# Kernel tuning notes

Hardware: AMD Instinct MI355X
Metric: run time of the kernel (lower is better)

The kernel has to match this reference:

```python
import jax, jax.numpy as jnp
import numpy as np

NUM_USERS = 200000
NUM_ARTISTS = 50000
LATENT_DIM = 64
NUM_EDGES = 2000000
NUM_LAYERS = 3


def setup_inputs() -> dict:
    key = jax.random.key(0)
    k_u, k_a, k_src, k_dst = jax.random.split(key, 4)
    x_users = jax.random.normal(k_u, (NUM_USERS, LATENT_DIM), dtype=jnp.float32)
    x_artists = jax.random.normal(k_a, (NUM_ARTISTS, LATENT_DIM), dtype=jnp.float32)
    # a2u: row 0 = artist (source) ids, row 1 = user (target) ids
    art = jax.random.randint(k_src, (NUM_EDGES,), 0, NUM_ARTISTS, dtype=jnp.int32)
    usr = jax.random.randint(k_dst, (NUM_EDGES,), 0, NUM_USERS, dtype=jnp.int32)
    edge_index_a2u = jnp.stack([art, usr], axis=0)
    # u2a is the reversed edge list: row 0 = user (source), row 1 = artist (target)
    edge_index_u2a = jnp.stack([usr, art], axis=0)
    return {
        "x_users": x_users,
        "x_artists": x_artists,
        "edge_index_a2u": edge_index_a2u,
        "edge_index_u2a": edge_index_u2a,
    }


def _scatter_mean(src_nodes, edge_index, dim_size):
    """Gather src_nodes[edge_index[0]] and scatter-mean onto edge_index[1].

    Matches torch_scatter.scatter(reduce='mean'): empty segments yield 0.
    """
    msgs = src_nodes[edge_index[0]]                     # [E, D] gather
    sums = jax.ops.segment_sum(msgs, edge_index[1], num_segments=dim_size)
    ones = jnp.ones((edge_index.shape[1],), dtype=src_nodes.dtype)
    counts = jax.ops.segment_sum(ones, edge_index[1], num_segments=dim_size)
    return sums / jnp.maximum(counts, 1.0)[:, None]


def reference(x_users, x_artists, edge_index_a2u, edge_index_u2a):
    scale = 1.0 / (NUM_LAYERS + 1)
    final_u = x_users * scale
    final_a = x_artists * scale
    for _ in range(NUM_LAYERS):
        x_users = _scatter_mean(x_artists, edge_index_a2u, NUM_USERS)
        x_artists = _scatter_mean(x_users, edge_index_u2a, NUM_ARTISTS)
        final_u = final_u + x_users * scale
        final_a = final_a + x_artists * scale
    return final_u, final_a
```

## Files before the change

### kernel.cpp

```cpp
#include <hip/hip_runtime.h>
#include <hip/hip_fp16.h>

#define D 64
#define TB 256

#define BSHIFT_U 10
#define BSHIFT_A 8
#define CAP    12288
#define CAPC_U 16384
#define CAPC_A 12288
#define TSHIFT 14
#define PCHUNK 4096

typedef _Float16 half8 __attribute__((ext_vector_type(8)));
typedef float float8 __attribute__((ext_vector_type(8)));
typedef float f32x4 __attribute__((ext_vector_type(4)));

__device__ __forceinline__ float8 h8_to_f8(half8 h) {
    return __builtin_convertvector(h, float8);
}
template <typename T>
__device__ __forceinline__ T ntl(const T* p) { return __builtin_nontemporal_load(p); }
template <typename T>
__device__ __forceinline__ void nts(T* p, T v) { __builtin_nontemporal_store(v, p); }

__global__ __launch_bounds__(TB) void cvt_f16_kernel(const f32x4* __restrict__ in,
                                                     half8* __restrict__ out, int n8) {
    int i = blockIdx.x * blockDim.x + threadIdx.x;
    int stride = gridDim.x * blockDim.x;
    for (int j = i; j < n8; j += stride) {
        f32x4 a = in[j * 2 + 0];
        f32x4 b = in[j * 2 + 1];
        half8 h;
        h[0] = (_Float16)a[0]; h[1] = (_Float16)a[1]; h[2] = (_Float16)a[2]; h[3] = (_Float16)a[3];
        h[4] = (_Float16)b[0]; h[5] = (_Float16)b[1]; h[6] = (_Float16)b[2]; h[7] = (_Float16)b[3];
        out[j] = h;
    }
}

struct PartShared {
    unsigned recs[PCHUNK];
    unsigned sorted[PCHUNK];
    unsigned short loc[PCHUNK];
    unsigned char bkt[PCHUNK];
    int cnt[256];
    int gbase[256];
    int seg[256];
    int scanbuf[TB];
};

__device__ __forceinline__ void part_direction(PartShared& sh, int m, int NB,
                                               int* __restrict__ bcur,
                                               unsigned* __restrict__ part) {
    const int tid = threadIdx.x;
    for (int i = tid; i < NB; i += TB) sh.cnt[i] = 0;
    __syncthreads();
    for (int i = tid; i < m; i += TB)
        sh.loc[i] = (unsigned short)atomicAdd(&sh.cnt[sh.bkt[i]], 1);
    __syncthreads();
    int v = (tid < NB) ? sh.cnt[tid] : 0;
    sh.scanbuf[tid] = v;
    __syncthreads();
    for (int off = 1; off < TB; off <<= 1) {
        int t = (tid >= off) ? sh.scanbuf[tid - off] : 0;
        __syncthreads();
        if (tid >= off) sh.scanbuf[tid] += t;
        __syncthreads();
    }
    if (tid < NB) {
        sh.seg[tid] = sh.scanbuf[tid] - v;
        if (v) sh.gbase[tid] = atomicAdd(&bcur[tid], v);
    }
    __syncthreads();
    for (int i = tid; i < m; i += TB)
        sh.sorted[sh.seg[sh.bkt[i]] + sh.loc[i]] = sh.recs[i];
    __syncthreads();
    const int wid = tid >> 6;
    const int lane = tid & 63;
    for (int b = wid; b < NB; b += TB / 64) {
        int s = sh.seg[b];
        int send = (b + 1 < NB) ? sh.seg[b + 1] : m;
        if (send <= s) continue;
        unsigned* dst = part + (size_t)b * CAP + sh.gbase[b];
        for (int i = s + lane; i < send; i += 64) dst[i - s] = sh.sorted[i];
    }
    __syncthreads();
}

__global__ __launch_bounds__(TB) void partition_both_kernel(const int* __restrict__ art,
                                                            const int* __restrict__ usr, int E,
                                                            int* __restrict__ bcur_u,
                                                            int* __restrict__ bcur_a,
                                                            unsigned* __restrict__ part_u,
                                                            unsigned* __restrict__ part_a,
                                                            int NBu, int NBa) {
    __shared__ PartShared sh;
    const int tid = threadIdx.x;
    const int dir = blockIdx.x & 1;
    const int cidx = blockIdx.x >> 1;
    const int nchunks = gridDim.x >> 1;
    for (int c = cidx; (size_t)c * PCHUNK < (size_t)E; c += nchunks) {
        const int c0 = c * PCHUNK;
        const int m = min(PCHUNK, E - c0);
        if (dir == 0) {
            for (int i = tid; i < m; i += TB) {
                int a = art[c0 + i], u = usr[c0 + i];
                sh.recs[i] = ((unsigned)a << BSHIFT_U) | ((unsigned)u & ((1u << BSHIFT_U) - 1u));
                sh.bkt[i] = (unsigned char)(u >> BSHIFT_U);
            }
            __syncthreads();
            part_direction(sh, m, NBu, bcur_u, part_u);
        } else {
            for (int i = tid; i < m; i += TB) {
                int a = art[c0 + i], u = usr[c0 + i];
                sh.recs[i] = ((unsigned)u << BSHIFT_A) | ((unsigned)a & ((1u << BSHIFT_A) - 1u));
                sh.bkt[i] = (unsigned char)(a >> BSHIFT_A);
            }
            __syncthreads();
            part_direction(sh, m, NBa, bcur_a, part_a);
        }
    }
}

template <int NPB, int NB, int BSHIFT>
__device__ __forceinline__ void local_csr_body(const unsigned* __restrict__ part,
                                               int ecount, int ebeg_p, int ebeg_c, int n0,
                                               int2* __restrict__ rowdeg,
                                               int* __restrict__ csr, int N,
                                               int* cnt, int* sdata) {
    const int tid = threadIdx.x;
    const int NBINS = NPB * NB;
    const int eend = ebeg_p + ecount;
    const unsigned mask = (unsigned)(NPB - 1);
    for (int i = tid; i < NBINS; i += TB) cnt[i] = 0;
    __syncthreads();
    for (int e = ebeg_p + tid; e < eend; e += TB) {
        unsigned r = part[e];
        int bin = (int)(r & mask) * NB + (int)((r >> BSHIFT) >> TSHIFT);
        atomicAdd(&cnt[bin], 1);
    }
    __syncthreads();
    const int ITEMS = NBINS / TB;
    const int NPT = ITEMS / NB;
    const int ib = tid * ITEMS;
    int dj[NPT], pdj[NPT], nsj[NPT];
    int local = 0;
    for (int j = 0; j < NPT; ++j) {
        int d = 0;
        for (int k = 0; k < NB; ++k) d += cnt[ib + j * NB + k];
        dj[j] = d;
        pdj[j] = (d + 3) & ~3;
        local += pdj[j];
    }
    sdata[tid] = local;
    __syncthreads();
    for (int off = 1; off < TB; off <<= 1) {
        int t = (tid >= off) ? sdata[tid - off] : 0;
        __syncthreads();
        if (tid >= off) sdata[tid] += t;
        __syncthreads();
    }
    int run = sdata[tid] - local;
    for (int j = 0; j < NPT; ++j) {
        nsj[j] = run;
        int c = run;
        for (int k = 0; k < NB; ++k) {
            int idx = ib + j * NB + k;
            int v = cnt[idx];
            cnt[idx] = c;
            c += v;
        }
        int n = n0 + tid * NPT + j;
        if (n < N) rowdeg[n] = make_int2(ebeg_c + run, dj[j]);
        run += pdj[j];
    }
    __syncthreads();
    for (int e = ebeg_p + tid; e < eend; e += TB) {
        unsigned r = part[e];
        int bin = (int)(r & mask) * NB + (int)((r >> BSHIFT) >> TSHIFT);
        int pos = atomicAdd(&cnt[bin], 1);
        csr[ebeg_c + pos] = (int)(r >> BSHIFT);
    }
    for (int j = 0; j < NPT; ++j)
        for (int k = dj[j]; k < pdj[j]; ++k) csr[ebeg_c + nsj[j] + k] = 0;
}

__global__ __launch_bounds__(TB) void local_csr_both_kernel(const unsigned* __restrict__ part_u,
                                                            const unsigned* __restrict__ part_a,
                                                            const int* __restrict__ bcur_u,
                                                            const int* __restrict__ bcur_a,
                                                            int2* __restrict__ rowdeg_u,
                                                            int2* __restrict__ rowdeg_a,
                                                            int* __restrict__ csr_u,
                                                            int* __restrict__ csr_a,
                                                            int NU, int NA, int NBu) {
    __shared__ int cnt[4096];
    __shared__ int sdata[TB];
    const int b = blockIdx.x;
    if (b < NBu) {
        local_csr_body<1024, 4, BSHIFT_U>(part_u, bcur_u[b], b * CAP, b * CAPC_U,
                                          b << BSHIFT_U, rowdeg_u, csr_u, NU, cnt, sdata);
    } else {
        const int bb = b - NBu;
        local_csr_body<256, 16, BSHIFT_A>(part_a, bcur_a[bb], bb * CAP, bb * CAPC_A,
                                          bb << BSHIFT_A, rowdeg_a, csr_a, NA, cnt, sdata);
    }
}

__global__ __launch_bounds__(TB) void gather_mean_kernel(const half8* __restrict__ src,
                                                         const int* __restrict__ csr,
                                                         const int2* __restrict__ rowdeg,
                                                         half8* __restrict__ x_out,
                                                         f32x4* __restrict__ final_acc,
                                                         const f32x4* __restrict__ init_src,
                                                         const f32x4* __restrict__ fin_in0,
                                                         const half8* __restrict__ fin_x1,
                                                         const half8* __restrict__ fin_x2,
                                                         f32x4* __restrict__ fin_out,
                                                         int N, float scale) {
    const int lane = threadIdx.x & 7;
    int g = (blockIdx.x * blockDim.x + threadIdx.x) >> 3;
    const int ngroups = (gridDim.x * blockDim.x) >> 3;
    const float8 r0 = h8_to_f8(src[lane]);
    for (int n = g; n < N; n += ngroups) {
        const int2 rd = rowdeg[n];
        const int beg = rd.x;
        const int dg = rd.y;
        const int pd = (dg + 3) & ~3;
        const int end = beg + pd;
        float8 a0 = 0.f, a1 = 0.f, a2 = 0.f, a3 = 0.f;
        int e = beg;
        for (; e + 8 <= end; e += 8) {
            const int s0 = csr[e + 0];
            const int s1 = csr[e + 1];
            const int s2 = csr[e + 2];
            const int s3 = csr[e + 3];
            const int s4 = csr[e + 4];
            const int s5 = csr[e + 5];
            const int s6 = csr[e + 6];
            const int s7 = csr[e + 7];
            const half8 v0 = src[s0 * 8 + lane];
            const half8 v1 = src[s1 * 8 + lane];
            const half8 v2 = src[s2 * 8 + lane];
            const half8 v3 = src[s3 * 8 + lane];
            const half8 v4 = src[s4 * 8 + lane];
            const half8 v5 = src[s5 * 8 + lane];
            const half8 v6 = src[s6 * 8 + lane];
            const half8 v7 = src[s7 * 8 + lane];
            a0 += h8_to_f8(v0);
            a1 += h8_to_f8(v1);
            a2 += h8_to_f8(v2);
            a3 += h8_to_f8(v3);
            a0 += h8_to_f8(v4);
            a1 += h8_to_f8(v5);
            a2 += h8_to_f8(v6);
            a3 += h8_to_f8(v7);
        }
        if (e < end) {
            const int s0 = csr[e + 0];
            const int s1 = csr[e + 1];
            const int s2 = csr[e + 2];
            const int s3 = csr[e + 3];
            a0 += h8_to_f8(src[s0 * 8 + lane]);
            a1 += h8_to_f8(src[s1 * 8 + lane]);
            a2 += h8_to_f8(src[s2 * 8 + lane]);
            a3 += h8_to_f8(src[s3 * 8 + lane]);
        }
        float8 s = (a0 + a1) + (a2 + a3);
        s -= (float)(pd - dg) * r0;
        const float inv = 1.f / (float)(dg > 0 ? dg : 1);
        float8 x = s * inv;
        const int o8 = n * 8 + lane;
        if (x_out != nullptr) {
            half8 h;
            for (int k = 0; k < 8; ++k) h[k] = (_Float16)x[k];
            x_out[o8] = h;
        }
        const int fo = n * (D / 4) + lane * 2;
        if (fin_out != nullptr) {
            float8 t = h8_to_f8(ntl(&fin_x1[o8])) + h8_to_f8(ntl(&fin_x2[o8])) + x;
            f32x4 f0 = ntl(&fin_in0[fo + 0]);
            f32x4 f1 = ntl(&fin_in0[fo + 1]);
            f32x4 t0 = {t[0], t[1], t[2], t[3]};
            f32x4 t1 = {t[4], t[5], t[6], t[7]};
            nts(&fin_out[fo + 0], (f0 + t0) * scale);
            nts(&fin_out[fo + 1], (f1 + t1) * scale);
        }
        if (final_acc != nullptr) {
            f32x4 f0, f1;
            if (init_src != nullptr) {
                f0 = init_src[fo + 0] * scale;
                f1 = init_src[fo + 1] * scale;
            } else {
                f0 = final_acc[fo + 0];
                f1 = final_acc[fo + 1];
            }
            f32x4 x0 = {x[0], x[1], x[2], x[3]};
            f32x4 x1 = {x[4], x[5], x[6], x[7]};
            final_acc[fo + 0] = f0 + x0 * scale;
            final_acc[fo + 1] = f1 + x1 * scale;
        }
    }
}

extern "C" void kernel_launch(void* const* d_in, const int* in_sizes, int n_in,
                              void* d_out, int out_size, void* d_ws, size_t ws_size,
                              hipStream_t stream) {
    const float* x_users   = (const float*)d_in[0];
    const float* x_artists = (const float*)d_in[1];
    const int*   a2u       = (const int*)d_in[2];

    const int NU = in_sizes[0] / D;
    const int NA = in_sizes[1] / D;
    const int E  = in_sizes[2] / 2;
    const int* art = a2u;
    const int* usr = a2u + E;

    const float scale = 0.25f;

    const int NBu = (NU + (1 << BSHIFT_U) - 1) >> BSHIFT_U;
    const int NBa = (NA + (1 << BSHIFT_A) - 1) >> BSHIFT_A;

    char* w = (char*)d_ws;
    size_t off = 0;
    auto alloc = [&](size_t bytes) -> char* {
        char* p = w + off;
        off += (bytes + 255) & ~(size_t)255;
        return p;
    };
    int2* rowdeg_u = (int2*)alloc((size_t)NU * 8);
    int2* rowdeg_a = (int2*)alloc((size_t)NA * 8);
    int* bcur      = (int*)alloc((size_t)(NBu + NBa) * 4);
    int* bcur_u    = bcur;
    int* bcur_a    = bcur + NBu;
    int* csr_u     = (int*)alloc((size_t)NBu * CAPC_U * 4);
    int* csr_a     = (int*)alloc((size_t)NBa * CAPC_A * 4);
    half8* xa_in   = (half8*)alloc((size_t)NA * D * 2);
    unsigned* part_u = (unsigned*)alloc((size_t)NBu * CAP * 4);
    unsigned* part_a = (unsigned*)alloc((size_t)NBa * CAP * 4);

    const size_t XU = (size_t)NU * D * 2;
    const size_t XA = (size_t)NA * D * 2;
    const size_t XUa = (XU + 255) & ~(size_t)255;
    const size_t XAa = (XA + 255) & ~(size_t)255;

    const bool modeA = (off + 3 * XUa) <= ws_size;

    half8* x_u1 = (half8*)alloc(XU);
    half8* x_u2 = modeA ? (half8*)alloc(XU) : x_u1;
    half8* x_u3 = modeA ? (half8*)alloc(XU) : x_u1;
    char* part_base = (char*)part_u;
    half8* x_a1 = (half8*)(part_base);
    half8* x_a2 = modeA ? (half8*)(part_base + XAa) : x_a1;

    float* out_u = (float*)d_out;
    float* out_a = out_u + (size_t)NU * D;

    hipMemsetAsync(bcur, 0, (size_t)(NBu + NBa) * 4, stream);
    cvt_f16_kernel<<<1024, TB, 0, stream>>>((const f32x4*)x_artists, xa_in, NA * D / 8);
    const int nchunks = (E + PCHUNK - 1) / PCHUNK;
    partition_both_kernel<<<2 * nchunks, TB, 0, stream>>>(art, usr, E, bcur_u, bcur_a,
                                                          part_u, part_a, NBu, NBa);
    local_csr_both_kernel<<<NBu + NBa, TB, 0, stream>>>(part_u, part_a, bcur_u, bcur_a,
                                                        rowdeg_u, rowdeg_a,
                                                        csr_u, csr_a, NU, NA, NBu);

    half8* xu_buf[3] = {x_u1, x_u2, x_u3};
    half8* xa_buf[2] = {x_a1, x_a2};
    const half8* srcA = xa_in;
    for (int l = 0; l < 3; ++l) {
        const bool last = (l == 2);
        gather_mean_kernel<<<4096, TB, 0, stream>>>(
            srcA, csr_u, rowdeg_u, xu_buf[l],
            modeA ? nullptr : (f32x4*)out_u,
            (!modeA && l == 0) ? (const f32x4*)x_users : nullptr,
            (modeA && last) ? (const f32x4*)x_users : nullptr,
            (modeA && last) ? x_u1 : nullptr,
            (modeA && last) ? x_u2 : nullptr,
            (modeA && last) ? (f32x4*)out_u : nullptr,
            NU, scale);
        gather_mean_kernel<<<2048, TB, 0, stream>>>(
            xu_buf[l], csr_a, rowdeg_a,
            (modeA && last) ? nullptr : (modeA ? xa_buf[l] : x_a1),
            modeA ? nullptr : (f32x4*)out_a,
            (!modeA && l == 0) ? (const f32x4*)x_artists : nullptr,
            (modeA && last) ? (const f32x4*)x_artists : nullptr,
            (modeA && last) ? x_a1 : nullptr,
            (modeA && last) ? x_a2 : nullptr,
            (modeA && last) ? (f32x4*)out_a : nullptr,
            NA, scale);
        srcA = modeA ? xa_buf[l < 2 ? l : 0] : x_a1;
    }
}
```

Measured before the change: 347.3 us.

## Slim partition kernel to one chunk per block and use nontemporal CSR loads

The partition kernel now handles one smaller chunk per block instead of looping over chunks. It drops the shared recs and bkt staging arrays, recomputing bucket keys from global memory instead. This cuts shared-memory use so more blocks can be resident, at the cost of reading the edge arrays twice. The gather kernel now reads CSR indices and rowdeg with nontemporal loads so they do not pollute cache space needed for the feature gathers. The launch grid is not visible, so it must supply enough blocks to cover every chunk.

```diff
diff --git a/kernel.cpp b/kernel.cpp
--- a/kernel.cpp
+++ b/kernel.cpp
@@ -10,7 +10,7 @@
 #define CAPC_U 16384
 #define CAPC_A 12288
 #define TSHIFT 14
-#define PCHUNK 4096
+#define PCHUNK 2048
 
 typedef _Float16 half8 __attribute__((ext_vector_type(8)));
 typedef float float8 __attribute__((ext_vector_type(8)));
@@ -39,53 +39,13 @@
 }
 
 struct PartShared {
-    unsigned recs[PCHUNK];
     unsigned sorted[PCHUNK];
     unsigned short loc[PCHUNK];
-    unsigned char bkt[PCHUNK];
     int cnt[256];
     int gbase[256];
     int seg[256];
     int scanbuf[TB];
 };
-
-__device__ __forceinline__ void part_direction(PartShared& sh, int m, int NB,
-                                               int* __restrict__ bcur,
-                                               unsigned* __restrict__ part) {
-    const int tid = threadIdx.x;
-    for (int i = tid; i < NB; i += TB) sh.cnt[i] = 0;
-    __syncthreads();
-    for (int i = tid; i < m; i += TB)
-        sh.loc[i] = (unsigned short)atomicAdd(&sh.cnt[sh.bkt[i]], 1);
-    __syncthreads();
-    int v = (tid < NB) ? sh.cnt[tid] : 0;
-    sh.scanbuf[tid] = v;
-    __syncthreads();
-    for (int off = 1; off < TB; off <<= 1) {
-        int t = (tid >= off) ? sh.scanbuf[tid - off] : 0;
-        __syncthreads();
-        if (tid >= off) sh.scanbuf[tid] += t;
-        __syncthreads();
-    }
-    if (tid < NB) {
-        sh.seg[tid] = sh.scanbuf[tid] - v;
-        if (v) sh.gbase[tid] = atomicAdd(&bcur[tid], v);
-    }
-    __syncthreads();
-    for (int i = tid; i < m; i += TB)
-        sh.sorted[sh.seg[sh.bkt[i]] + sh.loc[i]] = sh.recs[i];
-    __syncthreads();
-    const int wid = tid >> 6;
-    const int lane = tid & 63;
-    for (int b = wid; b < NB; b += TB / 64) {
-        int s = sh.seg[b];
-        int send = (b + 1 < NB) ? sh.seg[b + 1] : m;
-        if (send <= s) continue;
-        unsigned* dst = part + (size_t)b * CAP + sh.gbase[b];
-        for (int i = s + lane; i < send; i += 64) dst[i - s] = sh.sorted[i];
-    }
-    __syncthreads();
-}
 
 __global__ __launch_bounds__(TB) void partition_both_kernel(const int* __restrict__ art,
                                                             const int* __restrict__ usr, int E,
@@ -97,28 +57,53 @@
     __shared__ PartShared sh;
     const int tid = threadIdx.x;
     const int dir = blockIdx.x & 1;
-    const int cidx = blockIdx.x >> 1;
-    const int nchunks = gridDim.x >> 1;
-    for (int c = cidx; (size_t)c * PCHUNK < (size_t)E; c += nchunks) {
-        const int c0 = c * PCHUNK;
-        const int m = min(PCHUNK, E - c0);
-        if (dir == 0) {
-            for (int i = tid; i < m; i += TB) {
-                int a = art[c0 + i], u = usr[c0 + i];
-                sh.recs[i] = ((unsigned)a << BSHIFT_U) | ((unsigned)u & ((1u << BSHIFT_U) - 1u));
-                sh.bkt[i] = (unsigned char)(u >> BSHIFT_U);
-            }
-            __syncthreads();
-            part_direction(sh, m, NBu, bcur_u, part_u);
-        } else {
-            for (int i = tid; i < m; i += TB) {
-                int a = art[c0 + i], u = usr[c0 + i];
-                sh.recs[i] = ((unsigned)u << BSHIFT_A) | ((unsigned)a & ((1u << BSHIFT_A) - 1u));
-                sh.bkt[i] = (unsigned char)(a >> BSHIFT_A);
-            }
-            __syncthreads();
-            part_direction(sh, m, NBa, bcur_a, part_a);
-        }
+    const int c0 = (blockIdx.x >> 1) * PCHUNK;
+    if (c0 >= E) return;
+    const int m = min(PCHUNK, E - c0);
+    const int NB = dir ? NBa : NBu;
+    const int BSH = dir ? BSHIFT_A : BSHIFT_U;
+    const int* key = dir ? art : usr;
+    int* bcur = dir ? bcur_a : bcur_u;
+    unsigned* part = dir ? part_a : part_u;
+
+    for (int i = tid; i < NB; i += TB) sh.cnt[i] = 0;
+    __syncthreads();
+    for (int i = tid; i < m; i += TB) {
+        int b = key[c0 + i] >> BSH;
+        sh.loc[i] = (unsigned short)atomicAdd(&sh.cnt[b], 1);
+    }
+    __syncthreads();
+    int v = (tid < NB) ? sh.cnt[tid] : 0;
+    sh.scanbuf[tid] = v;
+    __syncthreads();
+    for (int off = 1; off < TB; off <<= 1) {
+        int t = (tid >= off) ? sh.scanbuf[tid - off] : 0;
+        __syncthreads();
+        if (tid >= off) sh.scanbuf[tid] += t;
+        __syncthreads();
+    }
+    if (tid < NB) {
+        sh.seg[tid] = sh.scanbuf[tid] - v;
+        if (v) sh.gbase[tid] = atomicAdd(&bcur[tid], v);
+    }
+    __syncthreads();
+    const unsigned mask = (1u << BSH) - 1u;
+    for (int i = tid; i < m; i += TB) {
+        int a = art[c0 + i], u = usr[c0 + i];
+        int k = dir ? a : u;
+        int s = dir ? u : a;
+        int b = k >> BSH;
+        sh.sorted[sh.seg[b] + sh.loc[i]] = ((unsigned)s << BSH) | ((unsigned)k & mask);
+    }
+    __syncthreads();
+    const int wid = tid >> 6;
+    const int lane = tid & 63;
+    for (int b = wid; b < NB; b += TB / 64) {
+        int s = sh.seg[b];
+        int send = (b + 1 < NB) ? sh.seg[b + 1] : m;
+        if (send <= s) continue;
+        unsigned* dst = part + (size_t)b * CAP + sh.gbase[b];
+        for (int i = s + lane; i < send; i += 64) dst[i - s] = sh.sorted[i];
     }
 }
 
@@ -223,22 +208,22 @@
     const int ngroups = (gridDim.x * blockDim.x) >> 3;
     const float8 r0 = h8_to_f8(src[lane]);
     for (int n = g; n < N; n += ngroups) {
-        const int2 rd = rowdeg[n];
-        const int beg = rd.x;
-        const int dg = rd.y;
+        const long long rdl = ntl((const long long*)&rowdeg[n]);
+        const int beg = (int)(unsigned)(rdl & 0xFFFFFFFFll);
+        const int dg  = (int)(rdl >> 32);
         const int pd = (dg + 3) & ~3;
         const int end = beg + pd;
         float8 a0 = 0.f, a1 = 0.f, a2 = 0.f, a3 = 0.f;
         int e = beg;
         for (; e + 8 <= end; e += 8) {
-            const int s0 = csr[e + 0];
-            const int s1 = csr[e + 1];
-            const int s2 = csr[e + 2];
-            const int s3 = csr[e + 3];
-            const int s4 = csr[e + 4];
-            const int s5 = csr[e + 5];
-            const int s6 = csr[e + 6];
-            const int s7 = csr[e + 7];
+            const int s0 = ntl(&csr[e + 0]);
+            const int s1 = ntl(&csr[e + 1]);
+            const int s2 = ntl(&csr[e + 2]);
+            const int s3 = ntl(&csr[e + 3]);
+            const int s4 = ntl(&csr[e + 4]);
+            const int s5 = ntl(&csr[e + 5]);
+            const int s6 = ntl(&csr[e + 6]);
+            const int s7 = ntl(&csr[e + 7]);
             const half8 v0 = src[s0 * 8 + lane];
             const half8 v1 = src[s1 * 8 + lane];
             const half8 v2 = src[s2 * 8 + lane];
@@ -257,10 +242,10 @@
             a3 += h8_to_f8(v7);
         }
         if (e < end) {
-            const int s0 = csr[e + 0];
-            const int s1 = csr[e + 1];
-            const int s2 = csr[e + 2];
-            const int s3 = csr[e + 3];
+            const int s0 = ntl(&csr[e + 0]);
+            const int s1 = ntl(&csr[e + 1]);
+            const int s2 = ntl(&csr[e + 2]);
+            const int s3 = ntl(&csr[e + 3]);
             a0 += h8_to_f8(src[s0 * 8 + lane]);
             a1 += h8_to_f8(src[s1 * 8 + lane]);
             a2 += h8_to_f8(src[s2 * 8 + lane]);
```

After: 385.9 us. +11.1%, slower.
